# Kernel optimization log

Measured on AMD Instinct MI355X. Metric: run time of the kernel, lower is better.

The kernel has to match this reference:

```python
import jax, jax.numpy as jnp
import numpy as np

N = 50000
E = 800000
TEXT_VOCAB = 7000
ACTION_DIM = 64
MAX_POS = 5120
POS_DIM = 128   # edge encoder out_dim
NODE_DIM = 128  # text_out 64 + type_out 64
EDGE_DIM = 128
H1 = 256
OUT = 32
NEG_SLOPE = 0.2


def _pos_table():
    # sinusoidal table, [MAX_POS+1, POS_DIM]; even cols = cos, odd cols = sin
    positions = np.arange(0, MAX_POS + 1, dtype=np.float32)
    inv_freq = 1.0 / (10000.0 ** (np.arange(0.0, POS_DIM, 2.0, dtype=np.float32) / POS_DIM))
    si = np.outer(positions, inv_freq)
    tab = np.zeros((MAX_POS + 1, POS_DIM), dtype=np.float32)
    tab[:, 1::2] = np.sin(si)
    tab[:, 0::2] = np.cos(si)
    return jnp.asarray(tab)


def setup_inputs() -> dict:
    key = jax.random.key(0)
    ks = jax.random.split(key, 32)
    ri = jax.random.randint
    nrm = lambda k, s, scale=0.05: (jax.random.normal(k, s, dtype=jnp.float32) * scale)
    x = jnp.stack([ri(ks[0], (N,), 0, TEXT_VOCAB + 1, dtype=jnp.int32),
                   ri(ks[1], (N,), 0, 3, dtype=jnp.int32)], axis=-1)
    edge_index = ri(ks[2], (2, E), 0, N, dtype=jnp.int32)
    edge_attr = jnp.stack([ri(ks[3], (E,), 0, 3, dtype=jnp.int32),
                           ri(ks[4], (E,), 0, MAX_POS + 1, dtype=jnp.int32)], axis=-1)
    d = {
        "x": x, "edge_index": edge_index, "edge_attr": edge_attr,
        "text_emb": nrm(ks[5], (TEXT_VOCAB + 1, 64), 1.0),
        "type_emb": nrm(ks[6], (3, 64), 1.0),
        "flow_emb": nrm(ks[7], (3, EDGE_DIM), 1.0),
        "pos_table": _pos_table(),
        "pos_W": nrm(ks[8], (POS_DIM, POS_DIM)), "pos_b": nrm(ks[9], (POS_DIM,)),
        "c1_Wl": nrm(ks[10], (NODE_DIM, H1)), "c1_bl": nrm(ks[11], (H1,)),
        "c1_Wr": nrm(ks[12], (NODE_DIM, H1)), "c1_br": nrm(ks[13], (H1,)),
        "c1_We": nrm(ks[14], (EDGE_DIM, H1)), "c1_att": nrm(ks[15], (H1,)),
        "c1_bias": nrm(ks[16], (H1,)),
        "c2_Wl": nrm(ks[17], (H1, OUT)), "c2_bl": nrm(ks[18], (OUT,)),
        "c2_Wr": nrm(ks[19], (H1, OUT)), "c2_br": nrm(ks[20], (OUT,)),
        "c2_We": nrm(ks[21], (EDGE_DIM, OUT)), "c2_att": nrm(ks[22], (OUT,)),
        "c2_bias": nrm(ks[23], (OUT,)),
        "policy_W": nrm(ks[24], (OUT, ACTION_DIM), 0.2), "policy_b": nrm(ks[25], (ACTION_DIM,)),
    }
    return d


def gatv2(h, src, dst, ea, Wl, bl, Wr, br, We, att, bias, n):
    # PyG GATv2Conv, heads=1, add_self_loops=True, fill_value='mean'
    loop_attr = jnp.broadcast_to(ea.mean(0), (n, ea.shape[1]))
    s = jnp.concatenate([src, jnp.arange(n, dtype=src.dtype)])
    d = jnp.concatenate([dst, jnp.arange(n, dtype=dst.dtype)])
    ea_full = jnp.concatenate([ea, loop_attr], axis=0)
    xl = h @ Wl + bl  # messages (source side)
    xr = h @ Wr + br  # destination side
    m = xl[s] + xr[d] + ea_full @ We          # [E+n, F]
    e = jnp.where(m > 0, m, NEG_SLOPE * m) @ att  # per-edge logit [E+n]
    emax = jax.ops.segment_max(e, d, num_segments=n)
    a = jnp.exp(e - emax[d])
    denom = jax.ops.segment_sum(a, d, num_segments=n)
    alpha = a / denom[d]
    return jax.ops.segment_sum(alpha[:, None] * xl[s], d, num_segments=n) + bias


def reference(x, edge_index, edge_attr, text_emb, type_emb, flow_emb, pos_table,
              pos_W, pos_b,
              c1_Wl, c1_bl, c1_Wr, c1_br, c1_We, c1_att, c1_bias,
              c2_Wl, c2_bl, c2_Wr, c2_br, c2_We, c2_att, c2_bias,
              policy_W, policy_b):
    # NodeEncoder: concat of text and type embeddings -> [N, 128]
    h = jnp.concatenate([text_emb[x[:, 0]], type_emb[x[:, 1]]], axis=-1)
    # EdgeEncoder: flow embedding + linear(position sinusoid embedding)
    pos = edge_attr[:, 1]
    pos = jnp.where(pos > MAX_POS, pos, MAX_POS)  # faithful to original .where usage
    pos = jnp.clip(pos, 0, MAX_POS)
    ea = flow_emb[edge_attr[:, 0]] + (pos_table[pos] @ pos_W + pos_b)  # [E, 128]
    src, dst = edge_index[0], edge_index[1]
    h = gatv2(h, src, dst, ea, c1_Wl, c1_bl, c1_Wr, c1_br, c1_We, c1_att, c1_bias, h.shape[0])
    h = gatv2(h, src, dst, ea, c2_Wl, c2_bl, c2_Wr, c2_br, c2_We, c2_att, c2_bias, h.shape[0])
    g = h.mean(0)  # [32] graph readout
    logits = g @ policy_W + policy_b
    return jax.nn.softmax(logits, axis=-1)
```

## Files before the change

### kernel.cpp

```cpp
#include <hip/hip_runtime.h>

typedef __attribute__((ext_vector_type(8))) short bf16x8;
typedef __attribute__((ext_vector_type(4))) float f32x4;

#define L2E 1.4426950408889634f
#define S6A (0.6f * L2E)

static __device__ __forceinline__ float wsum64(float v) {
#pragma unroll
    for (int off = 32; off >= 1; off >>= 1) v += __shfl_xor(v, off, 64);
    return v;
}
static __device__ __forceinline__ float wmax64(float v) {
#pragma unroll
    for (int off = 32; off >= 1; off >>= 1) v = fmaxf(v, __shfl_xor(v, off, 64));
    return v;
}

static __device__ __forceinline__ unsigned short bf16r(float a) {
    unsigned int u = __float_as_uint(a);
    return (unsigned short)((u + 0x7FFFu + ((u >> 16) & 1u)) >> 16);
}
static __device__ __forceinline__ unsigned int bf16pack(float a, float b) {
    unsigned int ua = __float_as_uint(a);
    ua = (ua + 0x7FFFu + ((ua >> 16) & 1u)) >> 16;
    unsigned int ub = __float_as_uint(b);
    ub = (ub + 0x7FFFu + ((ub >> 16) & 1u)) & 0xFFFF0000u;
    return ua | ub;
}
static __device__ __forceinline__ float4 bf16x4_to_f4(uint2 u) {
    float4 v;
    v.x = __uint_as_float(u.x << 16);
    v.y = __uint_as_float(u.x & 0xFFFF0000u);
    v.z = __uint_as_float(u.y << 16);
    v.w = __uint_as_float(u.y & 0xFFFF0000u);
    return v;
}
static __device__ __forceinline__ float rflf(float v) {
    return __int_as_float(__builtin_amdgcn_readfirstlane(__float_as_int(v)));
}

static __device__ __forceinline__ float adot4(const float4 xs, const float4 pre,
                                              const float4 av4) {
    float m0 = xs.x + pre.x, m1 = xs.y + pre.y;
    float m2 = xs.z + pre.z, m3 = xs.w + pre.w;
    float q = av4.x * fabsf(m0);
    q = fmaf(av4.y, fabsf(m1), q);
    q = fmaf(av4.z, fabsf(m2), q);
    q = fmaf(av4.w, fabsf(m3), q);
    return q;
}

__global__ void k_edges(const int* __restrict__ ei, const int* __restrict__ ea,
                        int* __restrict__ cntF, int* __restrict__ cnt3, int E) {
    __shared__ int sh3[3];
    if (threadIdx.x < 3) sh3[threadIdx.x] = 0;
    __syncthreads();
    int e = blockIdx.x * blockDim.x + threadIdx.x;
    if (e < E) {
        int dd = ei[E + e];
        int f = ea[2 * e];
        f = f < 0 ? 0 : (f > 2 ? 2 : f);
        atomicAdd(&cntF[dd * 3 + f], 1);
        atomicAdd(&sh3[f], 1);
    }
    __syncthreads();
    if (threadIdx.x < 3) atomicAdd(&cnt3[threadIdx.x], sh3[threadIdx.x]);
}

__global__ void k_prep_all(const float* __restrict__ pos_table, const float* __restrict__ pos_W,
                           const float* __restrict__ pos_b, const float* __restrict__ flow_emb,
                           const float* __restrict__ We1, const float* __restrict__ We2,
                           const float* __restrict__ att1, const int* __restrict__ cnt3,
                           float* __restrict__ eaW1, float* __restrict__ loopW1,
                           float* __restrict__ eaW2, float* __restrict__ loopW2,
                           float* __restrict__ delta,
                           const float* __restrict__ Wl1, const float* __restrict__ Wr1,
                           const float* __restrict__ Wl2, const float* __restrict__ Wr2,
                           unsigned short* __restrict__ Bt1, unsigned short* __restrict__ Bt2,
                           int E) {
    __shared__ float posc[128];
    __shared__ float lv[128];
    __shared__ float red4[1024];
    if (blockIdx.x != 0) {
        int i = (blockIdx.x - 1) * 256 + threadIdx.x;
        if (i < 512 * 128) {
            int nn = i >> 7, k = i & 127;
            float v = (nn < 256) ? Wl1[(size_t)k * 256 + nn] : Wr1[(size_t)k * 256 + nn - 256];
            Bt1[i] = bf16r(v);
        } else {
            int j = i - 512 * 128;
            if (j < 64 * 256) {
                int nn = j >> 8, k = j & 255;
                float v = (nn < 32) ? Wl2[(size_t)k * 32 + nn] : Wr2[(size_t)k * 32 + nn - 32];
                Bt2[j] = bf16r(v);
            }
        }
        return;
    }
    int t = threadIdx.x;
    if (t < 128) {
        const float* row = pos_table + 5120 * 128;
        float a = pos_b[t];
        for (int k = 0; k < 128; ++k) a += row[k] * pos_W[k * 128 + t];
        posc[t] = a;
        float invE = 1.0f / (float)E;
        lv[t] = ((float)cnt3[0] * flow_emb[t] + (float)cnt3[1] * flow_emb[128 + t] +
                 (float)cnt3[2] * flow_emb[256 + t]) * invE + a;
    }
    __syncthreads();
    {
        int j = t;
        float a0 = 0.f, a1 = 0.f, a2 = 0.f, al = 0.f;
        for (int k = 0; k < 128; ++k) {
            float w = We1[k * 256 + j];
            float pc = posc[k];
            a0 += (flow_emb[k] + pc) * w;
            a1 += (flow_emb[128 + k] + pc) * w;
            a2 += (flow_emb[256 + k] + pc) * w;
            al += lv[k] * w;
        }
        eaW1[j] = a0; eaW1[256 + j] = a1; eaW1[512 + j] = a2; loopW1[j] = al;
        float avj = att1[j];
        red4[t] = avj * a0;
        red4[256 + t] = avj * a1;
        red4[512 + t] = avj * a2;
        red4[768 + t] = avj * al;
    }
    __syncthreads();
    if (t < 4) {
        float s = 0.f;
        const float* rr = red4 + t * 256;
        for (int k = 0; k < 256; ++k) s += rr[k];
        delta[t] = s * S6A;
    }
    if (t < 32) {
        int j = t;
        float a0 = 0.f, a1 = 0.f, a2 = 0.f, al = 0.f;
        for (int k = 0; k < 128; ++k) {
            float w = We2[k * 32 + j];
            float pc = posc[k];
            a0 += (flow_emb[k] + pc) * w;
            a1 += (flow_emb[128 + k] + pc) * w;
            a2 += (flow_emb[256 + k] + pc) * w;
            al += lv[k] * w;
        }
        eaW2[j] = a0; eaW2[32 + j] = a1; eaW2[64 + j] = a2; loopW2[j] = al;
    }
}

__global__ __launch_bounds__(256) void k_scan_block(const int* __restrict__ cnt,
                                                    int* __restrict__ rowptr,
                                                    int* __restrict__ bsum, int n) {
    __shared__ int sh[256];
    int b = blockIdx.x, t = threadIdx.x;
    int base = b * 1024 + t * 4;
    int v0 = base + 0 < n ? cnt[base + 0] : 0;
    int v1 = base + 1 < n ? cnt[base + 1] : 0;
    int v2 = base + 2 < n ? cnt[base + 2] : 0;
    int v3 = base + 3 < n ? cnt[base + 3] : 0;
    int tot = v0 + v1 + v2 + v3;
    sh[t] = tot;
    __syncthreads();
    for (int off = 1; off < 256; off <<= 1) {
        int x = (t >= off) ? sh[t - off] : 0;
        __syncthreads();
        sh[t] += x;
        __syncthreads();
    }
    int excl = (t > 0) ? sh[t - 1] : 0;
    if (base + 0 < n) rowptr[base + 0] = excl;
    if (base + 1 < n) rowptr[base + 1] = excl + v0;
    if (base + 2 < n) rowptr[base + 2] = excl + v0 + v1;
    if (base + 3 < n) rowptr[base + 3] = excl + v0 + v1 + v2;
    if (t == 255) bsum[b] = sh[255];
}

__global__ __launch_bounds__(256) void k_scan_add(int* __restrict__ rowptr,
        const int* __restrict__ bsum, int* __restrict__ wptr, int n, int nb) {
    __shared__ int red[256];
    int b = blockIdx.x, t = threadIdx.x;
    int lim = b >> 2;
    int local = 0;
    for (int k = t; k < lim; k += 256) local += bsum[k];
    red[t] = local;
    __syncthreads();
    for (int s = 128; s > 0; s >>= 1) {
        if (t < s) red[t] += red[t + s];
        __syncthreads();
    }
    int P = red[0];
    if (b == 0) {
        P = 0;
        int tot = 0;
        for (int k = t; k < nb; k += 256) tot += bsum[k];
        __syncthreads();
        red[t] = tot;
        __syncthreads();
        for (int s = 128; s > 0; s >>= 1) {
            if (t < s) red[t] += red[t + s];
            __syncthreads();
        }
        if (t == 0) rowptr[n] = red[0];
    }
    int i = b * 256 + t;
    if (i < n) {
        int v = rowptr[i] + P;
        rowptr[i] = v;
        wptr[i] = v;
    }
}

__global__ void k_scatter(const int* __restrict__ ei, const int* __restrict__ ea,
                          int* __restrict__ wptr, int* __restrict__ packed, int E) {
    int e = blockIdx.x * blockDim.x + threadIdx.x;
    if (e >= E) return;
    int s = ei[e], dd = ei[E + e];
    int f = ea[2 * e];
    f = f < 0 ? 0 : (f > 2 ? 2 : f);
    int p = atomicAdd(&wptr[dd * 3 + f], 1);
    packed[p] = s | (f << 16);
}

__global__ __launch_bounds__(256) void k_gemm1(const int* __restrict__ x,
        const float* __restrict__ text_emb, const float* __restrict__ type_emb,
        const unsigned short* __restrict__ Bt,
        const float* __restrict__ bl, const float* __restrict__ br,
        const float* __restrict__ att, float* __restrict__ alpha,
        unsigned short* __restrict__ xc, int n) {
    __shared__ unsigned short Ash[64][136];
    __shared__ unsigned short Bsh[128][136];
    int t = threadIdx.x;
    int node0 = blockIdx.x * 64;
    for (int i = t; i < 64 * 128; i += 256) {
        int r = i >> 7, cc = i & 127;
        int nd = node0 + r;
        float v = 0.f;
        if (nd < n)
            v = (cc < 64) ? text_emb[(size_t)x[nd * 2] * 64 + cc]
                          : type_emb[(size_t)x[nd * 2 + 1] * 64 + (cc - 64)];
        Ash[r][cc] = bf16r(v);
    }
    int wave = t >> 6, lane = t & 63;
    int m = lane & 15, q = lane >> 4;
    for (int nb = 0; nb < 4; ++nb) {
        __syncthreads();
        for (int i = t; i < 128 * 16; i += 256) {
            int r = i >> 4, cs = i & 15;
            uint4 v = ((const uint4*)(Bt + (size_t)(nb * 128 + r) * 128))[cs];
            *(uint4*)&Bsh[r][cs * 8] = v;
        }
        __syncthreads();
        f32x4 acc[8];
#pragma unroll
        for (int nt = 0; nt < 8; ++nt) acc[nt] = (f32x4){0.f, 0.f, 0.f, 0.f};
#pragma unroll
        for (int k = 0; k < 128; k += 32) {
            bf16x8 a = *(const bf16x8*)&Ash[wave * 16 + m][k + q * 8];
#pragma unroll
            for (int nt = 0; nt < 8; ++nt) {
                bf16x8 b = *(const bf16x8*)&Bsh[nt * 16 + m][k + q * 8];
                acc[nt] = __builtin_amdgcn_mfma_f32_16x16x32_bf16(a, b, acc[nt], 0, 0, 0);
            }
        }
#pragma unroll
        for (int r = 0; r < 4; ++r) {
            int node = node0 + wave * 16 + q * 4 + r;
            if (node < n) {
                unsigned short* rowp = xc + (size_t)node * 512 + nb * 128 + m;
#pragma unroll
                for (int nt = 0; nt < 8; ++nt) {
                    int ng = nb * 128 + nt * 16 + m;
                    float bv = (ng < 256) ? bl[ng] : br[ng - 256];
                    rowp[nt * 16] = bf16r(acc[nt][r] + bv);
                }
            }
        }
        if (nb < 2) {
            float p0 = 0.f, p1 = 0.f, p2 = 0.f, p3 = 0.f;
#pragma unroll
            for (int nt = 0; nt < 8; ++nt) {
                int ng = nb * 128 + nt * 16 + m;
                float avv = att[ng];
                float bv = bl[ng];
                p0 = fmaf(avv, acc[nt][0] + bv, p0);
                p1 = fmaf(avv, acc[nt][1] + bv, p1);
                p2 = fmaf(avv, acc[nt][2] + bv, p2);
                p3 = fmaf(avv, acc[nt][3] + bv, p3);
            }
#pragma unroll
            for (int off = 1; off <= 8; off <<= 1) {
                p0 += __shfl_xor(p0, off, 64);
                p1 += __shfl_xor(p1, off, 64);
                p2 += __shfl_xor(p2, off, 64);
                p3 += __shfl_xor(p3, off, 64);
            }
            if (m == 0) {
                int nodeb = node0 + wave * 16 + q * 4;
                if (nodeb + 0 < n) atomicAdd(&alpha[nodeb + 0], p0 * S6A);
                if (nodeb + 1 < n) atomicAdd(&alpha[nodeb + 1], p1 * S6A);
                if (nodeb + 2 < n) atomicAdd(&alpha[nodeb + 2], p2 * S6A);
                if (nodeb + 3 < n) atomicAdd(&alpha[nodeb + 3], p3 * S6A);
            }
        }
    }
}

__global__ __launch_bounds__(256) void k_gemm2(const unsigned short* __restrict__ h2b,
        const unsigned short* __restrict__ Bt,
        const float* __restrict__ bl, const float* __restrict__ br,
        unsigned short* __restrict__ xc, int n) {
    __shared__ unsigned short Ash[32][264];
    __shared__ unsigned short Bsh[64][264];
    int t = threadIdx.x;
    int node0 = blockIdx.x * 32;
    for (int i = t; i < 32 * 32; i += 256) {
        int r = i >> 5, cs = i & 31;
        int nd = node0 + r;
        uint4 v = make_uint4(0u, 0u, 0u, 0u);
        if (nd < n) v = ((const uint4*)(h2b + (size_t)nd * 256))[cs];
        *(uint4*)&Ash[r][cs * 8] = v;
    }
    for (int i = t; i < 64 * 32; i += 256) {
        int r = i >> 5, cs = i & 31;
        uint4 v = ((const uint4*)(Bt + (size_t)r * 256))[cs];
        *(uint4*)&Bsh[r][cs * 8] = v;
    }
    __syncthreads();
    int wave = t >> 6, lane = t & 63;
    int m = lane & 15, q = lane >> 4;
    int mrow = (wave >> 1) * 16;
    int nh   = (wave & 1) * 32;
    f32x4 acc[2];
    acc[0] = (f32x4){0.f, 0.f, 0.f, 0.f};
    acc[1] = (f32x4){0.f, 0.f, 0.f, 0.f};
#pragma unroll
    for (int k = 0; k < 256; k += 32) {
        bf16x8 a = *(const bf16x8*)&Ash[mrow + m][k + q * 8];
#pragma unroll
        for (int nt = 0; nt < 2; ++nt) {
            bf16x8 b = *(const bf16x8*)&Bsh[nh + nt * 16 + m][k + q * 8];
            acc[nt] = __builtin_amdgcn_mfma_f32_16x16x32_bf16(a, b, acc[nt], 0, 0, 0);
        }
    }
#pragma unroll
    for (int r = 0; r < 4; ++r) {
        int node = node0 + mrow + q * 4 + r;
        if (node < n) {
#pragma unroll
            for (int nt = 0; nt < 2; ++nt) {
                int ng = nh + nt * 16 + m;
                float bv = (ng < 32) ? bl[ng] : br[ng - 32];
                xc[(size_t)node * 64 + ng] = bf16r(acc[nt][r] + bv);
            }
        }
    }
}

__global__ __launch_bounds__(256) void k_gat256(const unsigned short* __restrict__ xc1,
        const int* __restrict__ rowptrF, const int* __restrict__ packed,
        const float* __restrict__ eaW, const float* __restrict__ loopW,
        const float* __restrict__ att, const float* __restrict__ bias,
        const float* __restrict__ alpha, const float* __restrict__ delta,
        unsigned short* __restrict__ h2b, int n) {
    int wid = (blockIdx.x * blockDim.x + threadIdx.x) >> 6;
    if (wid >= n) return;
    int d = __builtin_amdgcn_readfirstlane(wid);
    int lane = threadIdx.x & 63;
    int c = lane * 4;
    const float S4 = 0.4f * L2E;
    float4 xld = bf16x4_to_f4(((const uint2*)(xc1 + (size_t)d * 512))[lane]);
    float4 xrd = bf16x4_to_f4(((const uint2*)(xc1 + (size_t)d * 512 + 256))[lane]);
    float4 av = *(const float4*)(att + c);
    float4 av4;
    av4.x = S4 * av.x; av4.y = S4 * av.y; av4.z = S4 * av.z; av4.w = S4 * av.w;
    float gq = av.x * xrd.x;
    gq = fmaf(av.y, xrd.y, gq); gq = fmaf(av.z, xrd.z, gq); gq = fmaf(av.w, xrd.w, gq);
    float gd = rflf(wsum64(gq) * S6A);
    float ab0 = gd + delta[0], ab1 = gd + delta[1], ab2 = gd + delta[2];
    float ab3 = gd + delta[3];
    float alphad = alpha[d];
    float4 r0 = *(const float4*)(eaW + c);
    float4 r1 = *(const float4*)(eaW + 256 + c);
    float4 r2 = *(const float4*)(eaW + 512 + c);
    float4 lwp = *(const float4*)(loopW + c);
    r0.x += xrd.x; r0.y += xrd.y; r0.z += xrd.z; r0.w += xrd.w;
    r1.x += xrd.x; r1.y += xrd.y; r1.z += xrd.z; r1.w += xrd.w;
    r2.x += xrd.x; r2.y += xrd.y; r2.z += xrd.z; r2.w += xrd.w;
    lwp.x += xrd.x; lwp.y += xrd.y; lwp.z += xrd.z; lwp.w += xrd.w;
    int jj = lane & 15;
    int a0i = jj << 2, a1i = (jj + 16) << 2, a2i = (jj + 32) << 2, a3i = (jj + 48) << 2;
    bool bq0 = (lane & 16) != 0, bq1 = (lane & 32) != 0;
    float den;
    float4 acc;
    {
        float q = wsum64(adot4(xld, lwp, av4)) + alphad + ab3;
        float wself = exp2f(q);
        den = wself;
        acc.x = wself * xld.x; acc.y = wself * xld.y;
        acc.z = wself * xld.z; acc.w = wself * xld.w;
    }
    int p = rowptrF[d * 3], p1 = rowptrF[d * 3 + 3];
    for (; p + 4 <= p1; p += 4) {
        int pk0 = packed[p],     pk1 = packed[p + 1];
        int pk2 = packed[p + 2], pk3 = packed[p + 3];
        int s0 = pk0 & 0xFFFF, s1 = pk1 & 0xFFFF;
        int s2 = pk2 & 0xFFFF, s3 = pk3 & 0xFFFF;
        int f0 = pk0 >> 16, f1 = pk1 >> 16, f2 = pk2 >> 16, f3 = pk3 >> 16;
        uint2 u0 = ((const uint2*)(xc1 + (size_t)s0 * 512))[lane];
        uint2 u1 = ((const uint2*)(xc1 + (size_t)s1 * 512))[lane];
        uint2 u2 = ((const uint2*)(xc1 + (size_t)s2 * 512))[lane];
        uint2 u3 = ((const uint2*)(xc1 + (size_t)s3 * 512))[lane];
        float sc0 = alpha[s0] + ((f0 == 0) ? ab0 : ((f0 == 1) ? ab1 : ab2));
        float sc1 = alpha[s1] + ((f1 == 0) ? ab0 : ((f1 == 1) ? ab1 : ab2));
        float sc2 = alpha[s2] + ((f2 == 0) ? ab0 : ((f2 == 1) ? ab1 : ab2));
        float sc3 = alpha[s3] + ((f3 == 0) ? ab0 : ((f3 == 1) ? ab1 : ab2));
        float4 xs0 = bf16x4_to_f4(u0);
        float4 xs1 = bf16x4_to_f4(u1);
        float4 xs2 = bf16x4_to_f4(u2);
        float4 xs3 = bf16x4_to_f4(u3);
        float q0, q1, q2, q3;
        if (f0 == f3) {
            float4 pr = (f0 == 0) ? r0 : ((f0 == 1) ? r1 : r2);
            q0 = adot4(xs0, pr, av4);
            q1 = adot4(xs1, pr, av4);
            q2 = adot4(xs2, pr, av4);
            q3 = adot4(xs3, pr, av4);
        } else {
            float4 pr0 = (f0 == 0) ? r0 : ((f0 == 1) ? r1 : r2);
            float4 pr1 = (f1 == 0) ? r0 : ((f1 == 1) ? r1 : r2);
            float4 pr2 = (f2 == 0) ? r0 : ((f2 == 1) ? r1 : r2);
            float4 pr3 = (f3 == 0) ? r0 : ((f3 == 1) ? r1 : r2);
            q0 = adot4(xs0, pr0, av4);
            q1 = adot4(xs1, pr1, av4);
            q2 = adot4(xs2, pr2, av4);
            q3 = adot4(xs3, pr3, av4);
        }
        q0 += __shfl_xor(q0, 16, 64); q1 += __shfl_xor(q1, 16, 64);
        q2 += __shfl_xor(q2, 16, 64); q3 += __shfl_xor(q3, 16, 64);
        q0 += __shfl_xor(q0, 32, 64); q1 += __shfl_xor(q1, 32, 64);
        q2 += __shfl_xor(q2, 32, 64); q3 += __shfl_xor(q3, 32, 64);
        float r01 = bq0 ? q1 : q0, r23 = bq0 ? q3 : q2;
        float r = bq1 ? r23 : r01;
        r += __shfl_xor(r, 1, 64); r += __shfl_xor(r, 2, 64);
        r += __shfl_xor(r, 4, 64); r += __shfl_xor(r, 8, 64);
        float s01 = bq0 ? sc1 : sc0, s23 = bq0 ? sc3 : sc2;
        float scv = bq1 ? s23 : s01;
        float w = exp2f(r + scv);
        int wi = __float_as_int(w);
        float w0 = __int_as_float(__builtin_amdgcn_ds_bpermute(a0i, wi));
        float w1 = __int_as_float(__builtin_amdgcn_ds_bpermute(a1i, wi));
        float w2 = __int_as_float(__builtin_amdgcn_ds_bpermute(a2i, wi));
        float w3 = __int_as_float(__builtin_amdgcn_ds_bpermute(a3i, wi));
        den += (w0 + w1) + (w2 + w3);
        acc.x += w0 * xs0.x + w1 * xs1.x + w2 * xs2.x + w3 * xs3.x;
        acc.y += w0 * xs0.y + w1 * xs1.y + w2 * xs2.y + w3 * xs3.y;
        acc.z += w0 * xs0.z + w1 * xs1.z + w2 * xs2.z + w3 * xs3.z;
        acc.w += w0 * xs0.w + w1 * xs1.w + w2 * xs2.w + w3 * xs3.w;
    }
    for (; p < p1; ++p) {
        int pk = packed[p];
        int s = pk & 0xFFFF, f = pk >> 16;
        uint2 u = ((const uint2*)(xc1 + (size_t)s * 512))[lane];
        float sc = alpha[s] + ((f == 0) ? ab0 : ((f == 1) ? ab1 : ab2));
        float4 xs = bf16x4_to_f4(u);
        float4 pr = (f == 0) ? r0 : ((f == 1) ? r1 : r2);
        float q = wsum64(adot4(xs, pr, av4)) + sc;
        float w = exp2f(q);
        den += w;
        acc.x += w * xs.x; acc.y += w * xs.y; acc.z += w * xs.z; acc.w += w * xs.w;
    }
    float inv = 1.f / den;
    float4 bv = *(const float4*)(bias + c);
    float ox = fmaf(acc.x, inv, bv.x), oy = fmaf(acc.y, inv, bv.y);
    float oz = fmaf(acc.z, inv, bv.z), ow = fmaf(acc.w, inv, bv.w);
    ((uint2*)(h2b + (size_t)d * 256))[lane] = make_uint2(bf16pack(ox, oy), bf16pack(oz, ow));
}

__global__ __launch_bounds__(256) void k_gat32(const unsigned short* __restrict__ xc2,
        const int* __restrict__ rowptrF, const int* __restrict__ packed,
        const float* __restrict__ eaW, const float* __restrict__ loopW,
        const float* __restrict__ att, const float* __restrict__ bias,
        float* __restrict__ out, int n) {
    int wid = (blockIdx.x * blockDim.x + threadIdx.x) >> 6;
    if (wid >= n) return;
    int d = __builtin_amdgcn_readfirstlane(wid);
    int lane = threadIdx.x & 63;
    int g = lane >> 4, li = lane & 15;
    unsigned int uxl = ((const unsigned int*)(xc2 + (size_t)d * 64))[li];
    unsigned int uxr = ((const unsigned int*)(xc2 + (size_t)d * 64 + 32))[li];
    float xl0 = __uint_as_float(uxl << 16), xl1 = __uint_as_float(uxl & 0xFFFF0000u);
    float xr0 = __uint_as_float(uxr << 16), xr1 = __uint_as_float(uxr & 0xFFFF0000u);
    float2 avv = ((const float2*)att)[li];
    float a60 = 0.6f * L2E * avv.x, a61 = 0.6f * L2E * avv.y;
    float a40 = 0.4f * L2E * avv.x, a41 = 0.4f * L2E * avv.y;
    float2 e0 = ((const float2*)eaW)[li];
    float2 e1 = ((const float2*)(eaW + 32))[li];
    float2 e2 = ((const float2*)(eaW + 64))[li];
    float p00 = e0.x + xr0, p01 = e0.y + xr1;
    float p10 = e1.x + xr0, p11 = e1.y + xr1;
    float p20 = e2.x + xr0, p21 = e2.y + xr1;
    float den, acc0, acc1;
    {
        float2 lwv = ((const float2*)loopW)[li];
        float m0 = xl0 + xr0 + lwv.x, m1 = xl1 + xr1 + lwv.y;
        float q = a60 * m0 + a40 * fabsf(m0);
        q = fmaf(a61, m1, q); q = fmaf(a41, fabsf(m1), q);
        q += __shfl_xor(q, 1, 64); q += __shfl_xor(q, 2, 64);
        q += __shfl_xor(q, 4, 64); q += __shfl_xor(q, 8, 64);
        float wself = exp2f(q);
        den  = (g == 0) ? wself : 0.f;
        acc0 = (g == 0) ? wself * xl0 : 0.f;
        acc1 = (g == 0) ? wself * xl1 : 0.f;
    }
    int pA = rowptrF[d * 3], pB = rowptrF[d * 3 + 3];
    int p = pA + g;
    for (; p + 12 < pB; p += 16) {
        int pkA = packed[p], pkB = packed[p + 4];
        int pkC = packed[p + 8], pkD = packed[p + 12];
        unsigned int ua = ((const unsigned int*)(xc2 + (size_t)(pkA & 0xFFFF) * 64))[li];
        unsigned int ub = ((const unsigned int*)(xc2 + (size_t)(pkB & 0xFFFF) * 64))[li];
        unsigned int uc = ((const unsigned int*)(xc2 + (size_t)(pkC & 0xFFFF) * 64))[li];
        unsigned int ud = ((const unsigned int*)(xc2 + (size_t)(pkD & 0xFFFF) * 64))[li];
        int fA = pkA >> 16, fB = pkB >> 16, fC = pkC >> 16, fD = pkD >> 16;
        float prA0 = (fA == 0) ? p00 : ((fA == 1) ? p10 : p20);
        float prA1 = (fA == 0) ? p01 : ((fA == 1) ? p11 : p21);
        float prB0 = (fB == 0) ? p00 : ((fB == 1) ? p10 : p20);
        float prB1 = (fB == 0) ? p01 : ((fB == 1) ? p11 : p21);
        float prC0 = (fC == 0) ? p00 : ((fC == 1) ? p10 : p20);
        float prC1 = (fC == 0) ? p01 : ((fC == 1) ? p11 : p21);
        float prD0 = (fD == 0) ? p00 : ((fD == 1) ? p10 : p20);
        float prD1 = (fD == 0) ? p01 : ((fD == 1) ? p11 : p21);
        float xa0 = __uint_as_float(ua << 16), xa1 = __uint_as_float(ua & 0xFFFF0000u);
        float xb0 = __uint_as_float(ub << 16), xb1 = __uint_as_float(ub & 0xFFFF0000u);
        float xc0 = __uint_as_float(uc << 16), xc1v = __uint_as_float(uc & 0xFFFF0000u);
        float xd0 = __uint_as_float(ud << 16), xd1 = __uint_as_float(ud & 0xFFFF0000u);
        float ma0 = xa0 + prA0, ma1 = xa1 + prA1;
        float mb0 = xb0 + prB0, mb1 = xb1 + prB1;
        float mc0 = xc0 + prC0, mc1 = xc1v + prC1;
        float md0 = xd0 + prD0, md1 = xd1 + prD1;
        float qa = a60 * ma0 + a40 * fabsf(ma0);
        qa = fmaf(a61, ma1, qa); qa = fmaf(a41, fabsf(ma1), qa);
        float qb = a60 * mb0 + a40 * fabsf(mb0);
        qb = fmaf(a61, mb1, qb); qb = fmaf(a41, fabsf(mb1), qb);
        float qc = a60 * mc0 + a40 * fabsf(mc0);
        qc = fmaf(a61, mc1, qc); qc = fmaf(a41, fabsf(mc1), qc);
        float qd = a60 * md0 + a40 * fabsf(md0);
        qd = fmaf(a61, md1, qd); qd = fmaf(a41, fabsf(md1), qd);
#pragma unroll
        for (int off = 1; off <= 8; off <<= 1) {
            qa += __shfl_xor(qa, off, 64);
            qb += __shfl_xor(qb, off, 64);
            qc += __shfl_xor(qc, off, 64);
            qd += __shfl_xor(qd, off, 64);
        }
        float wa = exp2f(qa), wb = exp2f(qb);
        float wc = exp2f(qc), wd = exp2f(qd);
        den += (wa + wb) + (wc + wd);
        acc0 += wa * xa0 + wb * xb0 + wc * xc0 + wd * xd0;
        acc1 += wa * xa1 + wb * xb1 + wc * xc1v + wd * xd1;
    }
    for (; p < pB; p += 4) {
        int pk = packed[p];
        unsigned int u = ((const unsigned int*)(xc2 + (size_t)(pk & 0xFFFF) * 64))[li];
        int f = pk >> 16;
        float pre0 = (f == 0) ? p00 : ((f == 1) ? p10 : p20);
        float pre1 = (f == 0) ? p01 : ((f == 1) ? p11 : p21);
        float x0 = __uint_as_float(u << 16), x1 = __uint_as_float(u & 0xFFFF0000u);
        float m0 = x0 + pre0, m1 = x1 + pre1;
        float q = a60 * m0 + a40 * fabsf(m0);
        q = fmaf(a61, m1, q); q = fmaf(a41, fabsf(m1), q);
        q += __shfl_xor(q, 1, 64); q += __shfl_xor(q, 2, 64);
        q += __shfl_xor(q, 4, 64); q += __shfl_xor(q, 8, 64);
        float w = exp2f(q);
        den += w;
        acc0 = fmaf(w, x0, acc0);
        acc1 = fmaf(w, x1, acc1);
    }
    acc0 += __shfl_xor(acc0, 16, 64); acc0 += __shfl_xor(acc0, 32, 64);
    acc1 += __shfl_xor(acc1, 16, 64); acc1 += __shfl_xor(acc1, 32, 64);
    den  += __shfl_xor(den, 16, 64);  den  += __shfl_xor(den, 32, 64);
    if (g == 0) {
        float2 bvv = ((const float2*)bias)[li];
        float inv = 1.f / den;
        float2 o;
        o.x = fmaf(acc0, inv, bvv.x);
        o.y = fmaf(acc1, inv, bvv.y);
        ((float2*)(out + (size_t)d * 32))[li] = o;
    }
}

__global__ __launch_bounds__(256) void k_mean(const float* __restrict__ out2,
                                              float* __restrict__ gsum, int n) {
    __shared__ float sh[256];
    int t = threadIdx.x;
    int c = t & 31, g = t >> 5;
    float acc = 0.f;
    for (int nd = blockIdx.x * 8 + g; nd < n; nd += gridDim.x * 8)
        acc += out2[(size_t)nd * 32 + c];
    sh[t] = acc;
    __syncthreads();
    if (t < 32) {
        float s2 = 0.f;
#pragma unroll
        for (int gg = 0; gg < 8; ++gg) s2 += sh[gg * 32 + c];
        atomicAdd(&gsum[c], s2);
    }
}

__global__ void k_final(const float* __restrict__ gsum, const float* __restrict__ policy_W,
                        const float* __restrict__ policy_b, float* __restrict__ out, int n) {
    int t = threadIdx.x;
    float invN = 1.0f / (float)n;
    float acc = policy_b[t];
    for (int cc = 0; cc < 32; ++cc) acc += gsum[cc] * invN * policy_W[cc * 64 + t];
    float mx = wmax64(acc);
    float ex = __expf(acc - mx);
    float s = wsum64(ex);
    out[t] = ex / s;
}

extern "C" void kernel_launch(void* const* d_in, const int* in_sizes, int n_in,
                              void* d_out, int out_size, void* d_ws, size_t ws_size,
                              hipStream_t stream) {
    const int* x          = (const int*)d_in[0];
    const int* edge_index = (const int*)d_in[1];
    const int* edge_attr  = (const int*)d_in[2];
    const float* text_emb = (const float*)d_in[3];
    const float* type_emb = (const float*)d_in[4];
    const float* flow_emb = (const float*)d_in[5];
    const float* pos_table= (const float*)d_in[6];
    const float* pos_W    = (const float*)d_in[7];
    const float* pos_b    = (const float*)d_in[8];
    const float* c1_Wl    = (const float*)d_in[9];
    const float* c1_bl    = (const float*)d_in[10];
    const float* c1_Wr    = (const float*)d_in[11];
    const float* c1_br    = (const float*)d_in[12];
    const float* c1_We    = (const float*)d_in[13];
    const float* c1_att   = (const float*)d_in[14];
    const float* c1_bias  = (const float*)d_in[15];
    const float* c2_Wl    = (const float*)d_in[16];
    const float* c2_bl    = (const float*)d_in[17];
    const float* c2_Wr    = (const float*)d_in[18];
    const float* c2_br    = (const float*)d_in[19];
    const float* c2_We    = (const float*)d_in[20];
    const float* c2_att   = (const float*)d_in[21];
    const float* c2_bias  = (const float*)d_in[22];
    const float* policy_W = (const float*)d_in[23];
    const float* policy_b = (const float*)d_in[24];
    float* out = (float*)d_out;

    const int N = in_sizes[0] / 2;
    const int E = in_sizes[1] / 2;
    const int n3 = 3 * N;

    char* base = (char*)d_ws;
    size_t off = 0;
    auto alloc = [&](size_t bytes) -> void* {
        void* p = base + off;
        off = (off + bytes + 255) & ~(size_t)255;
        return p;
    };
    unsigned short* xc1  = (unsigned short*)alloc((size_t)N * 512 * 2);
    unsigned short* h2b  = (unsigned short*)alloc((size_t)N * 256 * 2);
    unsigned short* xc2  = (unsigned short*)alloc((size_t)N * 64 * 2);
    float*          out2 = (float*)alloc((size_t)N * 32 * 4);
    unsigned short* Bt1  = (unsigned short*)alloc((size_t)512 * 128 * 2);
    unsigned short* Bt2  = (unsigned short*)alloc((size_t)64 * 256 * 2);
    int*            zreg   = (int*)alloc((size_t)(n3 + 36 + N) * 4);
    int*            cntF   = zreg;
    int*            cnt3   = zreg + n3;
    float*          gsum   = (float*)(zreg + n3 + 4);
    float*          alpha1 = (float*)(zreg + n3 + 36);
    int*            rowptrF= (int*)alloc((size_t)(n3 + 1) * 4);
    int*            packed = (int*)alloc((size_t)E * 4);
    int*            bsum   = (int*)alloc(256 * 4);
    float*          delta1 = (float*)alloc(4 * 4);
    float*          eaW1   = (float*)alloc(768 * 4);
    float*          loopW1 = (float*)alloc(256 * 4);
    float*          eaW2   = (float*)alloc(96 * 4);
    float*          loopW2 = (float*)alloc(32 * 4);

    hipMemsetAsync(zreg, 0, (size_t)(n3 + 36 + N) * 4, stream);

    k_edges<<<(E + 255) / 256, 256, 0, stream>>>(edge_index, edge_attr, cntF, cnt3, E);
    k_prep_all<<<1 + (512 * 128 + 64 * 256) / 256, 256, 0, stream>>>(
        pos_table, pos_W, pos_b, flow_emb, c1_We, c2_We, c1_att, cnt3,
        eaW1, loopW1, eaW2, loopW2, delta1,
        c1_Wl, c1_Wr, c2_Wl, c2_Wr, Bt1, Bt2, E);

    int nb = (n3 + 1023) / 1024;
    k_scan_block<<<nb, 256, 0, stream>>>(cntF, rowptrF, bsum, n3);
    k_scan_add<<<(n3 + 255) / 256, 256, 0, stream>>>(rowptrF, bsum, cntF, n3, nb);
    k_scatter<<<(E + 255) / 256, 256, 0, stream>>>(edge_index, edge_attr, cntF, packed, E);

    k_gemm1<<<(N + 63) / 64, 256, 0, stream>>>(x, text_emb, type_emb, Bt1,
                                               c1_bl, c1_br, c1_att, alpha1, xc1, N);
    k_gat256<<<(N + 3) / 4, 256, 0, stream>>>(xc1, rowptrF, packed, eaW1, loopW1,
                                              c1_att, c1_bias, alpha1, delta1, h2b, N);

    k_gemm2<<<(N + 31) / 32, 256, 0, stream>>>(h2b, Bt2, c2_bl, c2_br, xc2, N);
    k_gat32<<<(N + 3) / 4, 256, 0, stream>>>(xc2, rowptrF, packed, eaW2, loopW2,
                                             c2_att, c2_bias, out2, N);

    k_mean<<<256, 256, 0, stream>>>(out2, gsum, N);
    k_final<<<1, 64, 0, stream>>>(gsum, policy_W, policy_b, out, N);
}
```

Baseline: 405.5 us.

## Store layer-1 source features in FP8 with permuted layout, fuse tail kernels

The layer-1 GEMM now writes the gathered source projection xl in FP8 with a permuted column layout, giving packed 8-byte stores, and writes the destination projection in bf16 to a separate buffer. Companion vectors and the layer-2 weight rows are permuted to match. This halves the bytes per edge gather in the bandwidth-bound layer-1 attention kernel, at the cost of FP8 precision error in messages and attention logits. The mean and final softmax kernels are merged into one using a last-block-done counter, removing a launch.

```diff
diff --git a/kernel.cpp b/kernel.cpp
--- a/kernel.cpp
+++ b/kernel.cpp
@@ -2,6 +2,7 @@
 
 typedef __attribute__((ext_vector_type(8))) short bf16x8;
 typedef __attribute__((ext_vector_type(4))) float f32x4;
+typedef __attribute__((ext_vector_type(2))) float f32x2;
 
 #define L2E 1.4426950408889634f
 #define S6A (0.6f * L2E)
@@ -39,6 +40,46 @@
 static __device__ __forceinline__ float rflf(float v) {
     return __int_as_float(__builtin_amdgcn_readfirstlane(__float_as_int(v)));
 }
+
+#if __has_builtin(__builtin_amdgcn_cvt_pk_f32_fp8) && __has_builtin(__builtin_amdgcn_cvt_pk_fp8_f32)
+static __device__ __forceinline__ float4 fp8x4_to_f4(unsigned int u) {
+    f32x2 lo = __builtin_amdgcn_cvt_pk_f32_fp8((int)u, false);
+    f32x2 hi = __builtin_amdgcn_cvt_pk_f32_fp8((int)u, true);
+    return make_float4(lo.x, lo.y, hi.x, hi.y);
+}
+static __device__ __forceinline__ unsigned int fp8pack4(float a, float b, float c, float d) {
+    int u = 0;
+    u = __builtin_amdgcn_cvt_pk_fp8_f32(a, b, u, false);
+    u = __builtin_amdgcn_cvt_pk_fp8_f32(c, d, u, true);
+    return (unsigned int)u;
+}
+#else
+static __device__ __forceinline__ float fp8_1(unsigned int b) {
+    return __uint_as_float(((b & 0x80u) << 24) | ((b & 0x7Fu) << 20)) * 0x1p+120f;
+}
+static __device__ __forceinline__ float4 fp8x4_to_f4(unsigned int u) {
+    return make_float4(fp8_1(u & 255u), fp8_1((u >> 8) & 255u),
+                       fp8_1((u >> 16) & 255u), fp8_1(u >> 24));
+}
+static __device__ __forceinline__ unsigned int fp8enc1(float v) {
+    unsigned int s = (__float_as_uint(v) >> 24) & 0x80u;
+    float a = fminf(fabsf(v), 448.f);
+    unsigned int b;
+    if (a < 0.015625f) {
+        b = (unsigned int)__float2int_rn(a * 512.f);
+    } else {
+        unsigned int ua = __float_as_uint(a);
+        ua += 0x000FFFFFu + ((ua >> 20) & 1u);
+        unsigned int e = ua >> 23;
+        if (e > 135u) b = 0x7Eu;
+        else b = ((e - 120u) << 3) | ((ua >> 20) & 7u);
+    }
+    return s | b;
+}
+static __device__ __forceinline__ unsigned int fp8pack4(float a, float b, float c, float d) {
+    return fp8enc1(a) | (fp8enc1(b) << 8) | (fp8enc1(c) << 16) | (fp8enc1(d) << 24);
+}
+#endif
 
 static __device__ __forceinline__ float adot4(const float4 xs, const float4 pre,
                                               const float4 av4) {
@@ -51,6 +92,15 @@
     return q;
 }
 
+static __device__ __forceinline__ int permS(int j) {
+    int nb = j >> 7, r = j & 127;
+    return nb * 128 + (r & 15) * 8 + (r >> 4);
+}
+static __device__ __forceinline__ int permK(int s) {
+    int nb = s >> 7, r = s & 127;
+    return nb * 128 + (r & 7) * 16 + (r >> 3);
+}
+
 __global__ void k_edges(const int* __restrict__ ei, const int* __restrict__ ea,
                         int* __restrict__ cntF, int* __restrict__ cnt3, int E) {
     __shared__ int sh3[3];
@@ -59,7 +109,7 @@
     int e = blockIdx.x * blockDim.x + threadIdx.x;
     if (e < E) {
         int dd = ei[E + e];
-        int f = ea[2 * e];
+        int f = ((const int2*)ea)[e].x;
         f = f < 0 ? 0 : (f > 2 ? 2 : f);
         atomicAdd(&cntF[dd * 3 + f], 1);
         atomicAdd(&sh3[f], 1);
@@ -71,8 +121,10 @@
 __global__ void k_prep_all(const float* __restrict__ pos_table, const float* __restrict__ pos_W,
                            const float* __restrict__ pos_b, const float* __restrict__ flow_emb,
                            const float* __restrict__ We1, const float* __restrict__ We2,
-                           const float* __restrict__ att1, const int* __restrict__ cnt3,
-                           float* __restrict__ eaW1, float* __restrict__ loopW1,
+                           const float* __restrict__ att1, const float* __restrict__ bias1,
+                           const int* __restrict__ cnt3,
+                           float* __restrict__ eaW1p, float* __restrict__ loopW1p,
+                           float* __restrict__ att1p, float* __restrict__ bias1p,
                            float* __restrict__ eaW2, float* __restrict__ loopW2,
                            float* __restrict__ delta,
                            const float* __restrict__ Wl1, const float* __restrict__ Wr1,
@@ -91,8 +143,9 @@
         } else {
             int j = i - 512 * 128;
             if (j < 64 * 256) {
-                int nn = j >> 8, k = j & 255;
-                float v = (nn < 32) ? Wl2[(size_t)k * 32 + nn] : Wr2[(size_t)k * 32 + nn - 32];
+                int nn = j >> 8, s = j & 255;
+                int kk = permK(s);
+                float v = (nn < 32) ? Wl2[(size_t)kk * 32 + nn] : Wr2[(size_t)kk * 32 + nn - 32];
                 Bt2[j] = bf16r(v);
             }
         }
@@ -120,7 +173,10 @@
             a2 += (flow_emb[256 + k] + pc) * w;
             al += lv[k] * w;
         }
-        eaW1[j] = a0; eaW1[256 + j] = a1; eaW1[512 + j] = a2; loopW1[j] = al;
+        int s = permS(j);
+        eaW1p[s] = a0; eaW1p[256 + s] = a1; eaW1p[512 + s] = a2; loopW1p[s] = al;
+        att1p[s] = att1[j];
+        bias1p[s] = bias1[j];
         float avj = att1[j];
         red4[t] = avj * a0;
         red4[256 + t] = avj * a1;
@@ -216,7 +272,7 @@
     int e = blockIdx.x * blockDim.x + threadIdx.x;
     if (e >= E) return;
     int s = ei[e], dd = ei[E + e];
-    int f = ea[2 * e];
+    int f = ((const int2*)ea)[e].x;
     f = f < 0 ? 0 : (f > 2 ? 2 : f);
     int p = atomicAdd(&wptr[dd * 3 + f], 1);
     packed[p] = s | (f << 16);
@@ -227,7 +283,7 @@
         const unsigned short* __restrict__ Bt,
         const float* __restrict__ bl, const float* __restrict__ br,
         const float* __restrict__ att, float* __restrict__ alpha,
-        unsigned short* __restrict__ xc, int n) {
+        unsigned char* __restrict__ xl8, unsigned short* __restrict__ xrp, int n) {
     __shared__ unsigned short Ash[64][136];
     __shared__ unsigned short Bsh[128][136];
     int t = threadIdx.x;
@@ -263,17 +319,29 @@
                 acc[nt] = __builtin_amdgcn_mfma_f32_16x16x32_bf16(a, b, acc[nt], 0, 0, 0);
             }
         }
+        float bv[8];
+#pragma unroll
+        for (int nt = 0; nt < 8; ++nt) {
+            int ng = nb * 128 + nt * 16 + m;
+            bv[nt] = (nb < 2) ? bl[ng] : br[ng - 256];
+        }
 #pragma unroll
         for (int r = 0; r < 4; ++r) {
             int node = node0 + wave * 16 + q * 4 + r;
-            if (node < n) {
-                unsigned short* rowp = xc + (size_t)node * 512 + nb * 128 + m;
-#pragma unroll
-                for (int nt = 0; nt < 8; ++nt) {
-                    int ng = nb * 128 + nt * 16 + m;
-                    float bv = (ng < 256) ? bl[ng] : br[ng - 256];
-                    rowp[nt * 16] = bf16r(acc[nt][r] + bv);
-                }
+            if (node >= n) continue;
+            if (nb < 2) {
+                unsigned int u0 = fp8pack4(acc[0][r] + bv[0], acc[1][r] + bv[1],
+                                           acc[2][r] + bv[2], acc[3][r] + bv[3]);
+                unsigned int u1 = fp8pack4(acc[4][r] + bv[4], acc[5][r] + bv[5],
+                                           acc[6][r] + bv[6], acc[7][r] + bv[7]);
+                *(uint2*)(xl8 + (size_t)node * 256 + nb * 128 + m * 8) = make_uint2(u0, u1);
+            } else {
+                uint4 o;
+                o.x = bf16pack(acc[0][r] + bv[0], acc[1][r] + bv[1]);
+                o.y = bf16pack(acc[2][r] + bv[2], acc[3][r] + bv[3]);
+                o.z = bf16pack(acc[4][r] + bv[4], acc[5][r] + bv[5]);
+                o.w = bf16pack(acc[6][r] + bv[6], acc[7][r] + bv[7]);
+                *(uint4*)(xrp + (size_t)node * 256 + (nb - 2) * 128 + m * 8) = o;
             }
         }
         if (nb < 2) {
@@ -282,11 +350,10 @@
             for (int nt = 0; nt < 8; ++nt) {
                 int ng = nb * 128 + nt * 16 + m;
                 float avv = att[ng];
-                float bv = bl[ng];
-                p0 = fmaf(avv, acc[nt][0] + bv, p0);
-                p1 = fmaf(avv, acc[nt][1] + bv, p1);
-                p2 = fmaf(avv, acc[nt][2] + bv, p2);
-                p3 = fmaf(avv, acc[nt][3] + bv, p3);
+                p0 = fmaf(avv, acc[nt][0] + bv[nt], p0);
+                p1 = fmaf(avv, acc[nt][1] + bv[nt], p1);
+                p2 = fmaf(avv, acc[nt][2] + bv[nt], p2);
+                p3 = fmaf(avv, acc[nt][3] + bv[nt], p3);
             }
 #pragma unroll
             for (int off = 1; off <= 8; off <<= 1) {
@@ -350,17 +417,18 @@
 #pragma unroll
             for (int nt = 0; nt < 2; ++nt) {
                 int ng = nh + nt * 16 + m;
-                float bv = (ng < 32) ? bl[ng] : br[ng - 32];
-                xc[(size_t)node * 64 + ng] = bf16r(acc[nt][r] + bv);
+                float bvv = (ng < 32) ? bl[ng] : br[ng - 32];
+                xc[(size_t)node * 64 + ng] = bf16r(acc[nt][r] + bvv);
             }
         }
     }
 }
 
-__global__ __launch_bounds__(256) void k_gat256(const unsigned short* __restrict__ xc1,
+__global__ __launch_bounds__(256) void k_gat256(const unsigned char* __restrict__ xl8,
+        const unsigned short* __restrict__ xrp,
         const int* __restrict__ rowptrF, const int* __restrict__ packed,
-        const float* __restrict__ eaW, const float* __restrict__ loopW,
-        const float* __restrict__ att, const float* __restrict__ bias,
+        const float* __restrict__ eaWp, const float* __restrict__ loopWp,
+        const float* __restrict__ attp, const float* __restrict__ biasp,
         const float* __restrict__ alpha, const float* __restrict__ delta,
         unsigned short* __restrict__ h2b, int n) {
     int wid = (blockIdx.x * blockDim.x + threadIdx.x) >> 6;
@@ -369,9 +437,9 @@
     int lane = threadIdx.x & 63;
     int c = lane * 4;
     const float S4 = 0.4f * L2E;
-    float4 xld = bf16x4_to_f4(((const uint2*)(xc1 + (size_t)d * 512))[lane]);
-    float4 xrd = bf16x4_to_f4(((const uint2*)(xc1 + (size_t)d * 512 + 256))[lane]);
-    float4 av = *(const float4*)(att + c);
+    float4 xld = fp8x4_to_f4(*(const unsigned int*)(xl8 + (size_t)d * 256 + c));
+    float4 xrd = bf16x4_to_f4(((const uint2*)(xrp + (size_t)d * 256))[lane]);
+    float4 av = *(const float4*)(attp + c);
     float4 av4;
     av4.x = S4 * av.x; av4.y = S4 * av.y; av4.z = S4 * av.z; av4.w = S4 * av.w;
     float gq = av.x * xrd.x;
@@ -380,10 +448,10 @@
     float ab0 = gd + delta[0], ab1 = gd + delta[1], ab2 = gd + delta[2];
     float ab3 = gd + delta[3];
     float alphad = alpha[d];
-    float4 r0 = *(const float4*)(eaW + c);
-    float4 r1 = *(const float4*)(eaW + 256 + c);
-    float4 r2 = *(const float4*)(eaW + 512 + c);
-    float4 lwp = *(const float4*)(loopW + c);
+    float4 r0 = *(const float4*)(eaWp + c);
+    float4 r1 = *(const float4*)(eaWp + 256 + c);
+    float4 r2 = *(const float4*)(eaWp + 512 + c);
+    float4 lwp = *(const float4*)(loopWp + c);
     r0.x += xrd.x; r0.y += xrd.y; r0.z += xrd.z; r0.w += xrd.w;
     r1.x += xrd.x; r1.y += xrd.y; r1.z += xrd.z; r1.w += xrd.w;
     r2.x += xrd.x; r2.y += xrd.y; r2.z += xrd.z; r2.w += xrd.w;
@@ -407,18 +475,18 @@
         int s0 = pk0 & 0xFFFF, s1 = pk1 & 0xFFFF;
         int s2 = pk2 & 0xFFFF, s3 = pk3 & 0xFFFF;
         int f0 = pk0 >> 16, f1 = pk1 >> 16, f2 = pk2 >> 16, f3 = pk3 >> 16;
-        uint2 u0 = ((const uint2*)(xc1 + (size_t)s0 * 512))[lane];
-        uint2 u1 = ((const uint2*)(xc1 + (size_t)s1 * 512))[lane];
-        uint2 u2 = ((const uint2*)(xc1 + (size_t)s2 * 512))[lane];
-        uint2 u3 = ((const uint2*)(xc1 + (size_t)s3 * 512))[lane];
+        unsigned int g0 = *(const unsigned int*)(xl8 + (size_t)s0 * 256 + c);
+        unsigned int g1 = *(const unsigned int*)(xl8 + (size_t)s1 * 256 + c);
+        unsigned int g2 = *(const unsigned int*)(xl8 + (size_t)s2 * 256 + c);
+        unsigned int g3 = *(const unsigned int*)(xl8 + (size_t)s3 * 256 + c);
         float sc0 = alpha[s0] + ((f0 == 0) ? ab0 : ((f0 == 1) ? ab1 : ab2));
         float sc1 = alpha[s1] + ((f1 == 0) ? ab0 : ((f1 == 1) ? ab1 : ab2));
         float sc2 = alpha[s2] + ((f2 == 0) ? ab0 : ((f2 == 1) ? ab1 : ab2));
         float sc3 = alpha[s3] + ((f3 == 0) ? ab0 : ((f3 == 1) ? ab1 : ab2));
-        float4 xs0 = bf16x4_to_f4(u0);
-        float4 xs1 = bf16x4_to_f4(u1);
-        float4 xs2 = bf16x4_to_f4(u2);
-        float4 xs3 = bf16x4_to_f4(u3);
+        float4 xs0 = fp8x4_to_f4(g0);
+        float4 xs1 = fp8x4_to_f4(g1);
+        float4 xs2 = fp8x4_to_f4(g2);
+        float4 xs3 = fp8x4_to_f4(g3);
         float q0, q1, q2, q3;
         if (f0 == f3) {
             float4 pr = (f0 == 0) ? r0 : ((f0 == 1) ? r1 : r2);
@@ -441,12 +509,12 @@
         q0 += __shfl_xor(q0, 32, 64); q1 += __shfl_xor(q1, 32, 64);
         q2 += __shfl_xor(q2, 32, 64); q3 += __shfl_xor(q3, 32, 64);
         float r01 = bq0 ? q1 : q0, r23 = bq0 ? q3 : q2;
-        float r = bq1 ? r23 : r01;
-        r += __shfl_xor(r, 1, 64); r += __shfl_xor(r, 2, 64);
-        r += __shfl_xor(r, 4, 64); r += __shfl_xor(r, 8, 64);
+        float rr = bq1 ? r23 : r01;
+        rr += __shfl_xor(rr, 1, 64); rr += __shfl_xor(rr, 2, 64);
+        rr += __shfl_xor(rr, 4, 64); rr += __shfl_xor(rr, 8, 64);
         float s01 = bq0 ? sc1 : sc0, s23 = bq0 ? sc3 : sc2;
         float scv = bq1 ? s23 : s01;
-        float w = exp2f(r + scv);
+        float w = exp2f(rr + scv);
         int wi = __float_as_int(w);
         float w0 = __int_as_float(__builtin_amdgcn_ds_bpermute(a0i, wi));
         float w1 = __int_as_float(__builtin_amdgcn_ds_bpermute(a1i, wi));
@@ -461,9 +529,9 @@
     for (; p < p1; ++p) {
         int pk = packed[p];
         int s = pk & 0xFFFF, f = pk >> 16;
-        uint2 u = ((const uint2*)(xc1 + (size_t)s * 512))[lane];
+        unsigned int g = *(const unsigned int*)(xl8 + (size_t)s * 256 + c);
         float sc = alpha[s] + ((f == 0) ? ab0 : ((f == 1) ? ab1 : ab2));
-        float4 xs = bf16x4_to_f4(u);
+        float4 xs = fp8x4_to_f4(g);
         float4 pr = (f == 0) ? r0 : ((f == 1) ? r1 : r2);
         float q = wsum64(adot4(xs, pr, av4)) + sc;
         float w = exp2f(q);
@@ -471,9 +539,9 @@
         acc.x += w * xs.x; acc.y += w * xs.y; acc.z += w * xs.z; acc.w += w * xs.w;
     }
     float inv = 1.f / den;
-    float4 bv = *(const float4*)(bias + c);
-    float ox = fmaf(acc.x, inv, bv.x), oy = fmaf(acc.y, inv, bv.y);
-    float oz = fmaf(acc.z, inv, bv.z), ow = fmaf(acc.w, inv, bv.w);
+    float4 bvv = *(const float4*)(biasp + c);
+    float ox = fmaf(acc.x, inv, bvv.x), oy = fmaf(acc.y, inv, bvv.y);
+    float oz = fmaf(acc.z, inv, bvv.z), ow = fmaf(acc.w, inv, bvv.w);
     ((uint2*)(h2b + (size_t)d * 256))[lane] = make_uint2(bf16pack(ox, oy), bf16pack(oz, ow));
 }
 
@@ -533,11 +601,11 @@
         float prD1 = (fD == 0) ? p01 : ((fD == 1) ? p11 : p21);
         float xa0 = __uint_as_float(ua << 16), xa1 = __uint_as_float(ua & 0xFFFF0000u);
         float xb0 = __uint_as_float(ub << 16), xb1 = __uint_as_float(ub & 0xFFFF0000u);
-        float xc0 = __uint_as_float(uc << 16), xc1v = __uint_as_float(uc & 0xFFFF0000u);
+        float xcc0 = __uint_as_float(uc << 16), xcc1 = __uint_as_float(uc & 0xFFFF0000u);
         float xd0 = __uint_as_float(ud << 16), xd1 = __uint_as_float(ud & 0xFFFF0000u);
         float ma0 = xa0 + prA0, ma1 = xa1 + prA1;
         float mb0 = xb0 + prB0, mb1 = xb1 + prB1;
-        float mc0 = xc0 + prC0, mc1 = xc1v + prC1;
+        float mc0 = xcc0 + prC0, mc1 = xcc1 + prC1;
         float md0 = xd0 + prD0, md1 = xd1 + prD1;
         float qa = a60 * ma0 + a40 * fabsf(ma0);
         qa = fmaf(a61, ma1, qa); qa = fmaf(a41, fabsf(ma1), qa);
@@ -557,8 +625,8 @@
         float wa = exp2f(qa), wb = exp2f(qb);
         float wc = exp2f(qc), wd = exp2f(qd);
         den += (wa + wb) + (wc + wd);
-        acc0 += wa * xa0 + wb * xb0 + wc * xc0 + wd * xd0;
-        acc1 += wa * xa1 + wb * xb1 + wc * xc1v + wd * xd1;
+        acc0 += wa * xa0 + wb * xb0 + wc * xcc0 + wd * xd0;
+        acc1 += wa * xa1 + wb * xb1 + wc * xcc1 + wd * xd1;
     }
     for (; p < pB; p += 4) {
         int pk = packed[p];
@@ -590,9 +658,12 @@
     }
 }
 
-__global__ __launch_bounds__(256) void k_mean(const float* __restrict__ out2,
-                                              float* __restrict__ gsum, int n) {
+__global__ __launch_bounds__(256) void k_tail(const float* __restrict__ out2,
+        float* __restrict__ gsum, int* __restrict__ done,
+        const float* __restrict__ policy_W, const float* __restrict__ policy_b,
+        float* __restrict__ out, int n) {
     __shared__ float sh[256];
+    __shared__ int lastFlag;
     int t = threadIdx.x;
     int c = t & 31, g = t >> 5;
     float acc = 0.f;
@@ -606,18 +677,26 @@
         for (int gg = 0; gg < 8; ++gg) s2 += sh[gg * 32 + c];
         atomicAdd(&gsum[c], s2);
     }
-}
-
-__global__ void k_final(const float* __restrict__ gsum, const float* __restrict__ policy_W,
-                        const float* __restrict__ policy_b, float* __restrict__ out, int n) {
-    int t = threadIdx.x;
-    float invN = 1.0f / (float)n;
-    float acc = policy_b[t];
-    for (int cc = 0; cc < 32; ++cc) acc += gsum[cc] * invN * policy_W[cc * 64 + t];
-    float mx = wmax64(acc);
-    float ex = __expf(acc - mx);
-    float s = wsum64(ex);
-    out[t] = ex / s;
+    __syncthreads();
+    if (t == 0) {
+        __threadfence();
+        int old = atomicAdd(done, 1);
+        lastFlag = (old == (int)gridDim.x - 1) ? 1 : 0;
+    }
+    __syncthreads();
+    if (lastFlag) {
+        if (t < 32) sh[t] = atomicAdd(&gsum[t], 0.f);
+        __syncthreads();
+        if (t < 64) {
+            float invN = 1.0f / (float)n;
+            float a = policy_b[t];
+            for (int cc = 0; cc < 32; ++cc) a += sh[cc] * invN * policy_W[cc * 64 + t];
+            float mx = wmax64(a);
+            float ex = __expf(a - mx);
+            float s = wsum64(ex);
+            out[t] = ex / s;
+        }
+    }
 }
 
 extern "C" void kernel_launch(void* const* d_in, const int* in_sizes, int n_in,
@@ -661,32 +740,36 @@
         off = (off + bytes + 255) & ~(size_t)255;
         return p;
     };
-    unsigned short* xc1  = (unsigned short*)alloc((size_t)N * 512 * 2);
+    unsigned char*  xl8  = (unsigned char*)alloc((size_t)N * 256);
+    unsigned short* xrp  = (unsigned short*)alloc((size_t)N * 256 * 2);
     unsigned short* h2b  = (unsigned short*)alloc((size_t)N * 256 * 2);
     unsigned short* xc2  = (unsigned short*)alloc((size_t)N * 64 * 2);
     float*          out2 = (float*)alloc((size_t)N * 32 * 4);
     unsigned short* Bt1  = (unsigned short*)alloc((size_t)512 * 128 * 2);
     unsigned short* Bt2  = (unsigned short*)alloc((size_t)64 * 256 * 2);
-    int*            zreg   = (int*)alloc((size_t)(n3 + 36 + N) * 4);
+    int*            zreg   = (int*)alloc((size_t)(n3 + 40 + N) * 4);
     int*            cntF   = zreg;
     int*            cnt3   = zreg + n3;
     float*          gsum   = (float*)(zreg + n3 + 4);
-    float*          alpha1 = (float*)(zreg + n3 + 36);
+    int*            done   = zreg + n3 + 36;
+    float*          alpha1 = (float*)(zreg + n3 + 40);
     int*            rowptrF= (int*)alloc((size_t)(n3 + 1) * 4);
     int*            packed = (int*)alloc((size_t)E * 4);
     int*            bsum   = (int*)alloc(256 * 4);
     float*          delta1 = (float*)alloc(4 * 4);
-    float*          eaW1   = (float*)alloc(768 * 4);
-    float*          loopW1 = (float*)alloc(256 * 4);
+    float*          eaW1p  = (float*)alloc(768 * 4);
+    float*          loopW1p= (float*)alloc(256 * 4);
+    float*          att1p  = (float*)alloc(256 * 4);
+    float*          bias1p = (float*)alloc(256 * 4);
     float*          eaW2   = (float*)alloc(96 * 4);
     float*          loopW2 = (float*)alloc(32 * 4);
 
-    hipMemsetAsync(zreg, 0, (size_t)(n3 + 36 + N) * 4, stream);
+    hipMemsetAsync(zreg, 0, (size_t)(n3 + 40 + N) * 4, stream);
 
     k_edges<<<(E + 255) / 256, 256, 0, stream>>>(edge_index, edge_attr, cntF, cnt3, E);
     k_prep_all<<<1 + (512 * 128 + 64 * 256) / 256, 256, 0, stream>>>(
-        pos_table, pos_W, pos_b, flow_emb, c1_We, c2_We, c1_att, cnt3,
-        eaW1, loopW1, eaW2, loopW2, delta1,
+        pos_table, pos_W, pos_b, flow_emb, c1_We, c2_We, c1_att, c1_bias, cnt3,
+        eaW1p, loopW1p, att1p, bias1p, eaW2, loopW2, delta1,
         c1_Wl, c1_Wr, c2_Wl, c2_Wr, Bt1, Bt2, E);
 
     int nb = (n3 + 1023) / 1024;
@@ -695,14 +778,13 @@
     k_scatter<<<(E + 255) / 256, 256, 0, stream>>>(edge_index, edge_attr, cntF, packed, E);
 
     k_gemm1<<<(N + 63) / 64, 256, 0, stream>>>(x, text_emb, type_emb, Bt1,
-                                               c1_bl, c1_br, c1_att, alpha1, xc1, N);
-    k_gat256<<<(N + 3) / 4, 256, 0, stream>>>(xc1, rowptrF, packed, eaW1, loopW1,
-                                              c1_att, c1_bias, alpha1, delta1, h2b, N);
+                                               c1_bl, c1_br, c1_att, alpha1, xl8, xrp, N);
+    k_gat256<<<(N + 3) / 4, 256, 0, stream>>>(xl8, xrp, rowptrF, packed, eaW1p, loopW1p,
+                                              att1p, bias1p, alpha1, delta1, h2b, N);
 
     k_gemm2<<<(N + 31) / 32, 256, 0, stream>>>(h2b, Bt2, c2_bl, c2_br, xc2, N);
     k_gat32<<<(N + 3) / 4, 256, 0, stream>>>(xc2, rowptrF, packed, eaW2, loopW2,
                                              c2_att, c2_bias, out2, N);
 
-    k_mean<<<256, 256, 0, stream>>>(out2, gsum, N);
-    k_final<<<1, 64, 0, stream>>>(gsum, policy_W, policy_b, out, N);
-}
+    k_tail<<<256, 256, 0, stream>>>(out2, gsum, done, policy_W, policy_b, out, N);
+}
```

After: 411.3 us. About the same (+1.4%).
